# Kernel optimization log

Hardware: AMD Instinct MI355X
Metric: run time of the kernel (lower is better)

The kernel has to match this reference:

```python
import jax, jax.numpy as jnp
import numpy as np

N = 50000   # nodes
E = 600000  # edges (both relations mixed)
D = 128     # in_features == out_features


def _gcn(x, W, b, row, col, w, n):
    """PyG GCNConv: add self-loops (weight 1), symmetric normalization, linear, aggregate, bias.
    Edges with w==0 contribute nothing to degree or messages (== masked subgraph)."""
    idx = jnp.arange(n)
    srow = jnp.concatenate([row, idx])
    scol = jnp.concatenate([col, idx])
    sw = jnp.concatenate([w, jnp.ones((n,), x.dtype)])
    deg = jax.ops.segment_sum(sw, scol, num_segments=n)                 # [n]
    dinv = jnp.where(deg > 0, jax.lax.rsqrt(jnp.maximum(deg, 1e-12)), 0.0)
    norm = dinv[srow] * sw * dinv[scol]                                 # [E+n]
    h = x @ W                                                           # [n, D]
    out = jax.ops.segment_sum(h[srow] * norm[:, None], scol, num_segments=n)
    return out + b


def setup_inputs() -> dict:
    key = jax.random.key(0)
    ks = jax.random.split(key, 12)
    s_in = 1.0 / np.sqrt(D)
    s_g = 1.0 / np.sqrt(3 * D)
    return {
        "x": jax.random.normal(ks[0], (N, D), dtype=jnp.float32),
        "edge_index": jax.random.randint(ks[1], (2, E), 0, N, dtype=jnp.int64),
        "edge_type": jax.random.randint(ks[2], (E,), 0, 2, dtype=jnp.int64),
        "W_sl": jax.random.normal(ks[3], (D, D), dtype=jnp.float32) * s_in,
        "b_sl": jnp.zeros((D,), jnp.float32),
        "W0": jax.random.normal(ks[4], (D, D), dtype=jnp.float32) * s_in,
        "b0": jnp.zeros((D,), jnp.float32),
        "W1": jax.random.normal(ks[5], (D, D), dtype=jnp.float32) * s_in,
        "b1": jnp.zeros((D,), jnp.float32),
        "W_g": jax.random.normal(ks[6], (3 * D, D), dtype=jnp.float32) * s_g,
        "b_g": jnp.zeros((D,), jnp.float32),
    }


def reference(x, edge_index, edge_type, W_sl, b_sl, W0, b0, W1, b1, W_g, b_g):
    n = x.shape[0]
    row, col = edge_index[0], edge_index[1]
    x_x = x @ W_sl + b_sl                                   # self-loop linear
    w0 = (edge_type == 0).astype(x.dtype)
    w1 = (edge_type == 1).astype(x.dtype)
    x_n = _gcn(x, W0, b0, row, col, w0, n)                  # relation 0 GCN
    x_d = _gcn(x, W1, b1, row, col, w1, n)                  # relation 1 GCN
    gat_raw = jax.nn.softmax(jnp.concatenate([x_x, x_n, x_d], axis=1) @ W_g + b_g, axis=-1)
    gat = jnp.cumsum(gat_raw, axis=-1)                      # ordered-neuron gate
    return x_d[:, ::-1] * gat + x_x + x_n
```

## Files before the change

### kernel.cpp

```cpp
#include <hip/hip_runtime.h>
#include <hip/hip_bf16.h>
#include <hip/hip_fp16.h>
#include <math.h>


typedef __attribute__((ext_vector_type(8))) short bf16x8;
typedef __attribute__((ext_vector_type(4))) float f32x4;
typedef __attribute__((ext_vector_type(8))) unsigned short ushort8;

__device__ inline float b2f(unsigned short u) {
  return __uint_as_float(((unsigned)u) << 16);
}
__device__ inline unsigned short f2bf(float f) {
  __hip_bfloat16 b = __float2bfloat16(f);
  return *reinterpret_cast<unsigned short*>(&b);
}

__global__ __launch_bounds__(256) void zero_deg(int4* __restrict__ deg4, int n4) {
  int i = blockIdx.x * 256 + threadIdx.x;
  if (i < n4) deg4[i] = make_int4(0, 0, 0, 0);
}

__global__ __launch_bounds__(256) void pack_count(const float* __restrict__ Wsl,
                                                  const float* __restrict__ W0,
                                                  const float* __restrict__ W1,
                                                  const float* __restrict__ Wg,
                                                  unsigned short* __restrict__ Wp3,
                                                  unsigned short* __restrict__ Wgp,
                                                  const int* __restrict__ col,
                                                  const int* __restrict__ etype,
                                                  int* __restrict__ deg,
                                                  int* __restrict__ erank, int E, int n) {
  if (blockIdx.x < 48) {
    int tid = blockIdx.x * 256 + threadIdx.x;
    if (tid < 6144) {
      int z = tid / 2048, r = tid % 2048;
      int lane = r & 63, idx = r >> 6;
      int kf = idx & 3, ct = idx >> 2;
      const float* W = (z == 0) ? Wsl : (z == 1) ? W0 : W1;
      unsigned short* dst = Wp3 + (size_t)z * 16384 + (size_t)r * 8;
      int krow = kf * 32 + (lane >> 4) * 8;
      int ccol = ct * 16 + (lane & 15);
#pragma unroll
      for (int j = 0; j < 8; ++j) dst[j] = f2bf(W[(size_t)(krow + j) * 128 + ccol]);
    } else {
      int r = tid - 6144;
      int lane = r & 63, idx = r >> 6;
      int kf = idx % 12, ct = idx / 12;
      unsigned short* dst = Wgp + (size_t)r * 8;
      int krow = kf * 32 + (lane >> 4) * 8;
      int ccol = ct * 16 + (lane & 15);
#pragma unroll
      for (int j = 0; j < 8; ++j) dst[j] = f2bf(Wg[(size_t)(krow + j) * 128 + ccol]);
    }
  } else {
    int e = (blockIdx.x - 48) * 256 + threadIdx.x;
    if (e >= E) return;
    int rk = atomicAdd(&deg[(size_t)etype[e] * n + col[e]], 1);
    erank[e] = rk;
  }
}

__global__ __launch_bounds__(256) void scan1(const int* __restrict__ deg,
                                             int* __restrict__ partials, int n2) {
  int tid = threadIdx.x;
  int base = blockIdx.x * 2048 + tid * 8;
  int s = 0;
#pragma unroll
  for (int k = 0; k < 8; ++k) {
    int i = base + k;
    if (i < n2) s += deg[i];
  }
  __shared__ int sb[256];
  sb[tid] = s;
  __syncthreads();
  for (int o = 128; o; o >>= 1) {
    if (tid < o) sb[tid] += sb[tid + o];
    __syncthreads();
  }
  if (tid == 0) partials[blockIdx.x] = sb[0];
}

__global__ __launch_bounds__(256) void scan3b(const int* __restrict__ partials,
                                              const int* __restrict__ deg,
                                              int* __restrict__ row_start,
                                              float* __restrict__ dinv, int n2, int nb) {
  __shared__ int sb[256];
  __shared__ int ex[256];
  int tid = threadIdx.x;
  int pv = (tid < nb) ? partials[tid] : 0;
  sb[tid] = pv;
  __syncthreads();
  for (int o = 1; o < 256; o <<= 1) {
    int t = (tid >= o) ? sb[tid - o] : 0;
    __syncthreads();
    sb[tid] += t;
    __syncthreads();
  }
  ex[tid] = sb[tid] - pv;
  __syncthreads();
  int base = ex[blockIdx.x];
  __syncthreads();

  int bstart = blockIdx.x * 2048 + tid * 8;
  int v[8];
  int s = 0;
#pragma unroll
  for (int k = 0; k < 8; ++k) {
    int i = bstart + k;
    v[k] = (i < n2) ? deg[i] : 0;
    s += v[k];
    if (i < n2) dinv[i] = rsqrtf((float)v[k] + 1.0f);
  }
  sb[tid] = s;
  __syncthreads();
  for (int o = 1; o < 256; o <<= 1) {
    int t = (tid >= o) ? sb[tid - o] : 0;
    __syncthreads();
    sb[tid] += t;
    __syncthreads();
  }
  int run = base + (sb[tid] - s);
#pragma unroll
  for (int k = 0; k < 8; ++k) {
    int i = bstart + k;
    if (i < n2) {
      row_start[i] = run;
      run += v[k];
    }
  }
}

__global__ __launch_bounds__(256) void gemm3_fill(
    const float* __restrict__ x, const unsigned short* __restrict__ Wp3,
    const float* __restrict__ bsl, unsigned short* __restrict__ hx,
    unsigned short* __restrict__ h0, unsigned short* __restrict__ h1,
    const int* __restrict__ row, const int* __restrict__ col,
    const int* __restrict__ etype, const int* __restrict__ erank,
    const int* __restrict__ row_start, const float* __restrict__ dinv,
    unsigned int* __restrict__ ebuf, int n, int E, int gb) {
  __shared__ unsigned short xs[64 * 136];
  __shared__ __align__(16) unsigned short Bs[2][4096];
  int tid = threadIdx.x;
  if ((int)blockIdx.x >= gb) {
    int e = (blockIdx.x - gb) * 256 + tid;
    if (e >= E) return;
    int r = row[e], c = col[e], t = etype[e];
    int b = t * n + c;
    float nrm = dinv[t * n + r] * dinv[b];
    int pos = row_start[b] + erank[e];
    unsigned int rec = (unsigned int)(r & 0xFFFF) |
                       ((unsigned int)__half_as_ushort(__float2half_rn(nrm)) << 16);
    ebuf[pos] = rec;
    return;
  }
  int row0 = blockIdx.x * 64;
  {
    const float4* xg = (const float4*)(x + (size_t)row0 * 128);
    int maxv = (n - row0) * 32;
#pragma unroll
    for (int i = 0; i < 8; ++i) {
      int idx = tid + i * 256;
      float4 v = {0.f, 0.f, 0.f, 0.f};
      if (idx < maxv) v = xg[idx];
      int rr = idx >> 5, c4 = idx & 31;
      ushort4 u;
      u.x = f2bf(v.x);
      u.y = f2bf(v.y);
      u.z = f2bf(v.z);
      u.w = f2bf(v.w);
      *(ushort4*)&xs[rr * 136 + c4 * 4] = u;
    }
    int u = tid;
#pragma unroll
    for (int r = 0; r < 2; ++r, u += 256) {
      int ct = u >> 6, ll = u & 63;
      *(ushort8*)&Bs[0][u * 8] = *(const ushort8*)(Wp3 + ((size_t)(ct * 4) * 64 + ll) * 8);
    }
  }
  __syncthreads();
  int w = tid >> 6;
  int l = tid & 63;
  int q = l >> 4;
  int c = l & 15;
  bf16x8 af[4];
#pragma unroll
  for (int kf = 0; kf < 4; ++kf)
    af[kf] = *(const bf16x8*)&xs[(w * 16 + c) * 136 + kf * 32 + q * 8];
  __syncthreads();

  f32x4 acc[8];
#pragma unroll
  for (int ct = 0; ct < 8; ++ct) acc[ct] = (f32x4){0.f, 0.f, 0.f, 0.f};
#pragma unroll
  for (int g = 0; g < 12; ++g) {
    int z = g >> 2, kf = g & 3;
    int cur = g & 1;
    if (g < 11) {
      int zn = (g + 1) >> 2, kfn = (g + 1) & 3;
      int u = tid;
#pragma unroll
      for (int r = 0; r < 2; ++r, u += 256) {
        int ct = u >> 6, ll = u & 63;
        *(ushort8*)&Bs[cur ^ 1][u * 8] = *(const ushort8*)(
            Wp3 + (size_t)zn * 16384 + ((size_t)(ct * 4 + kfn) * 64 + ll) * 8);
      }
    }
    bf16x8 a = af[kf];
#pragma unroll
    for (int ct = 0; ct < 8; ++ct)
      acc[ct] = __builtin_amdgcn_mfma_f32_16x16x32_bf16(
          a, *(const bf16x8*)&Bs[cur][(ct * 64 + l) * 8], acc[ct], 0, 0, 0);
    if (kf == 3) {
      unsigned short* h = (z == 0) ? hx : (z == 1) ? h0 : h1;
#pragma unroll
      for (int ct = 0; ct < 8; ++ct) {
        int fc = ct * 16 + c;
        float bias = (z == 0) ? bsl[fc] : 0.f;
#pragma unroll
        for (int i = 0; i < 4; ++i)
          xs[(w * 16 + q * 4 + i) * 136 + fc] = f2bf(acc[ct][i] + bias);
        acc[ct] = (f32x4){0.f, 0.f, 0.f, 0.f};
      }
      __syncthreads();
#pragma unroll
      for (int i = 0; i < 4; ++i) {
        int idx = tid + i * 256;
        int rr = idx >> 4, c8 = idx & 15;
        int gr = row0 + rr;
        if (gr < n)
          *(ushort8*)(h + (size_t)gr * 128 + c8 * 8) = *(const ushort8*)&xs[rr * 136 + c8 * 8];
      }
      __syncthreads();
    } else {
      __syncthreads();
    }
  }
}

__global__ __launch_bounds__(256) void gather2(const unsigned short* __restrict__ h0,
                                               const unsigned short* __restrict__ h1,
                                               const unsigned int* __restrict__ ebuf,
                                               const int* __restrict__ row_start,
                                               const int* __restrict__ deg,
                                               const float* __restrict__ dinv,
                                               const float* __restrict__ b0,
                                               const float* __restrict__ b1,
                                               unsigned short* __restrict__ xn,
                                               unsigned short* __restrict__ xd, int n) {
  int t = blockIdx.y;
  long long gid = (long long)blockIdx.x * 256 + threadIdx.x;
  int node = (int)(gid >> 3);
  if (node >= n) return;
  int sub = (int)(gid & 7);
  const ushort8* hp8 = (const ushort8*)(t ? h1 : h0);
  const float* bias = t ? b1 : b0;
  unsigned short* out = t ? xd : xn;
  const int* rs = row_start + (size_t)t * n;
  const int* dg = deg + (size_t)t * n;
  float di = dinv[(size_t)t * n + node];

  float accA[8], accB[8];
  float acc2A[8] = {0, 0, 0, 0, 0, 0, 0, 0}, acc2B[8] = {0, 0, 0, 0, 0, 0, 0, 0};
  {
    ushort8 sa = hp8[(size_t)node * 16 + sub * 2];
    ushort8 sbv = hp8[(size_t)node * 16 + sub * 2 + 1];
    float sl = di * di;
#pragma unroll
    for (int k = 0; k < 8; ++k) {
      accA[k] = fmaf(b2f(sa[k]), sl, bias[sub * 16 + k]);
      accB[k] = fmaf(b2f(sbv[k]), sl, bias[sub * 16 + 8 + k]);
    }
  }
  int s = rs[node];
  int e = s + dg[node];
  int j = s;
  for (; j + 3 < e; j += 4) {
    unsigned int r0 = ebuf[j], r1 = ebuf[j + 1], r2 = ebuf[j + 2], r3 = ebuf[j + 3];
    int i0 = (int)(r0 & 0xFFFFu), i1 = (int)(r1 & 0xFFFFu);
    int i2 = (int)(r2 & 0xFFFFu), i3 = (int)(r3 & 0xFFFFu);
    float n0 = __half2float(__ushort_as_half((unsigned short)(r0 >> 16)));
    float n1 = __half2float(__ushort_as_half((unsigned short)(r1 >> 16)));
    float n2 = __half2float(__ushort_as_half((unsigned short)(r2 >> 16)));
    float n3 = __half2float(__ushort_as_half((unsigned short)(r3 >> 16)));
    ushort8 v0a = hp8[(size_t)i0 * 16 + sub * 2];
    ushort8 v0b = hp8[(size_t)i0 * 16 + sub * 2 + 1];
    ushort8 v1a = hp8[(size_t)i1 * 16 + sub * 2];
    ushort8 v1b = hp8[(size_t)i1 * 16 + sub * 2 + 1];
    ushort8 v2a = hp8[(size_t)i2 * 16 + sub * 2];
    ushort8 v2b = hp8[(size_t)i2 * 16 + sub * 2 + 1];
    ushort8 v3a = hp8[(size_t)i3 * 16 + sub * 2];
    ushort8 v3b = hp8[(size_t)i3 * 16 + sub * 2 + 1];
#pragma unroll
    for (int k = 0; k < 8; ++k) {
      accA[k] = fmaf(b2f(v0a[k]), n0, accA[k]);
      accB[k] = fmaf(b2f(v0b[k]), n0, accB[k]);
      acc2A[k] = fmaf(b2f(v1a[k]), n1, acc2A[k]);
      acc2B[k] = fmaf(b2f(v1b[k]), n1, acc2B[k]);
      accA[k] = fmaf(b2f(v2a[k]), n2, accA[k]);
      accB[k] = fmaf(b2f(v2b[k]), n2, accB[k]);
      acc2A[k] = fmaf(b2f(v3a[k]), n3, acc2A[k]);
      acc2B[k] = fmaf(b2f(v3b[k]), n3, acc2B[k]);
    }
  }
  for (; j < e; ++j) {
    unsigned int r0 = ebuf[j];
    int i0 = (int)(r0 & 0xFFFFu);
    float n0 = __half2float(__ushort_as_half((unsigned short)(r0 >> 16)));
    ushort8 v0a = hp8[(size_t)i0 * 16 + sub * 2];
    ushort8 v0b = hp8[(size_t)i0 * 16 + sub * 2 + 1];
#pragma unroll
    for (int k = 0; k < 8; ++k) {
      accA[k] = fmaf(b2f(v0a[k]), n0, accA[k]);
      accB[k] = fmaf(b2f(v0b[k]), n0, accB[k]);
    }
  }
  ushort8 ua, ub;
#pragma unroll
  for (int k = 0; k < 8; ++k) {
    ua[k] = f2bf(accA[k] + acc2A[k]);
    ub[k] = f2bf(accB[k] + acc2B[k]);
  }
  ((ushort8*)out)[(size_t)node * 16 + sub * 2] = ua;
  ((ushort8*)out)[(size_t)node * 16 + sub * 2 + 1] = ub;
}

__global__ __launch_bounds__(256) void gate_combine(
    const unsigned short* __restrict__ hx, const unsigned short* __restrict__ xn,
    const unsigned short* __restrict__ xd, const unsigned short* __restrict__ Wgp,
    const float* __restrict__ bg, float* __restrict__ out, int n) {
  __shared__ __align__(16) unsigned short Bs[2][4096];
  int tid = threadIdx.x;
  int wv = tid >> 6;
  int l = tid & 63;
  int q = l >> 4;
  int c = l & 15;
  int row0 = blockIdx.x * 64 + wv * 16;
  int ar = row0 + c;
  if (ar > n - 1) ar = n - 1;
  bf16x8 af[12];
  {
    const unsigned short* p0 = hx + (size_t)ar * 128 + q * 8;
    const unsigned short* p1 = xn + (size_t)ar * 128 + q * 8;
    const unsigned short* p2 = xd + (size_t)ar * 128 + q * 8;
#pragma unroll
    for (int k = 0; k < 4; ++k) {
      af[k] = *(const bf16x8*)(p0 + k * 32);
      af[4 + k] = *(const bf16x8*)(p1 + k * 32);
      af[8 + k] = *(const bf16x8*)(p2 + k * 32);
    }
  }
  {
    int u = tid;
#pragma unroll
    for (int r = 0; r < 2; ++r, u += 256) {
      int ct = u >> 6, ll = u & 63;
      *(ushort8*)&Bs[0][u * 8] = *(const ushort8*)(Wgp + ((size_t)(ct * 12) * 64 + ll) * 8);
    }
  }
  __syncthreads();
  f32x4 acc[8];
#pragma unroll
  for (int ct = 0; ct < 8; ++ct) acc[ct] = (f32x4){0.f, 0.f, 0.f, 0.f};
#pragma unroll
  for (int kf = 0; kf < 12; ++kf) {
    int cur = kf & 1;
    if (kf < 11) {
      int u = tid;
#pragma unroll
      for (int r = 0; r < 2; ++r, u += 256) {
        int ct = u >> 6, ll = u & 63;
        *(ushort8*)&Bs[cur ^ 1][u * 8] =
            *(const ushort8*)(Wgp + ((size_t)(ct * 12 + kf + 1) * 64 + ll) * 8);
      }
    }
    bf16x8 a = af[kf];
#pragma unroll
    for (int ct = 0; ct < 8; ++ct)
      acc[ct] = __builtin_amdgcn_mfma_f32_16x16x32_bf16(
          a, *(const bf16x8*)&Bs[cur][(ct * 64 + l) * 8], acc[ct], 0, 0, 0);
    if (kf < 11) __syncthreads();
  }
#pragma unroll
  for (int ct = 0; ct < 8; ++ct) {
    float bgv = bg[ct * 16 + c];
#pragma unroll
    for (int i = 0; i < 4; ++i) acc[ct][i] += bgv;
  }
#pragma unroll
  for (int i = 0; i < 4; ++i) {
    float m = acc[0][i];
#pragma unroll
    for (int ct = 1; ct < 8; ++ct) m = fmaxf(m, acc[ct][i]);
#pragma unroll
    for (int o = 1; o < 16; o <<= 1) m = fmaxf(m, __shfl_xor(m, o));
    float e[8];
    float s = 0.f;
#pragma unroll
    for (int ct = 0; ct < 8; ++ct) {
      e[ct] = __expf(acc[ct][i] - m);
      s += e[ct];
    }
#pragma unroll
    for (int o = 1; o < 16; o <<= 1) s += __shfl_xor(s, o);
    float inv = 1.0f / s;
    int gr = row0 + q * 4 + i;
    float run = 0.f;
#pragma unroll
    for (int ct = 0; ct < 8; ++ct) {
      float p = e[ct];
#pragma unroll
      for (int o = 1; o < 16; o <<= 1) {
        float t = __shfl_up(p, o);
        if (c >= o) p += t;
      }
      float T = __shfl(p, q * 16 + 15);
      float gat = (run + p) * inv;
      run += T;
      int f = ct * 16 + c;
      if (gr < n) {
        size_t gb = (size_t)gr * 128;
        float xxv = b2f(hx[gb + f]);
        float xnv = b2f(xn[gb + f]);
        float xdv = b2f(xd[gb + 127 - f]);
        out[gb + f] = fmaf(xdv, gat, xxv + xnv);
      }
    }
  }
}

extern "C" void kernel_launch(void* const* d_in, const int* in_sizes, int n_in,
                              void* d_out, int out_size, void* d_ws, size_t ws_size,
                              hipStream_t stream) {
  const float* x = (const float*)d_in[0];
  const int* eidx = (const int*)d_in[1];
  const int* etype = (const int*)d_in[2];
  const float* Wsl = (const float*)d_in[3];
  const float* bsl = (const float*)d_in[4];
  const float* W0 = (const float*)d_in[5];
  const float* b0 = (const float*)d_in[6];
  const float* W1 = (const float*)d_in[7];
  const float* b1 = (const float*)d_in[8];
  const float* Wg = (const float*)d_in[9];
  const float* bg = (const float*)d_in[10];
  int n = in_sizes[0] / 128;
  int E = in_sizes[2];
  const int* row = eidx;
  const int* col = eidx + E;
  int n2 = 2 * n;

  char* w = (char*)d_ws;
  int* deg = (int*)w;             w += (size_t)n2 * 4;
  float* dinv = (float*)w;        w += (size_t)n2 * 4;
  int* row_start = (int*)w;       w += (size_t)n2 * 4;
  int* partials = (int*)w;        w += 1024;
  unsigned int* ebuf = (unsigned int*)w;  w += (size_t)E * 4;
  int* erank = (int*)w;           w += (size_t)E * 4;
  unsigned short* Wp3 = (unsigned short*)w;  w += 3 * 128 * 128 * 2;
  unsigned short* Wgp = (unsigned short*)w;  w += 384 * 128 * 2;
  unsigned short* hx = (unsigned short*)w;   w += (size_t)n * 128 * 2;
  unsigned short* h0 = (unsigned short*)w;   w += (size_t)n * 128 * 2;
  unsigned short* h1 = (unsigned short*)w;   w += (size_t)n * 128 * 2;
  unsigned short* xn = (unsigned short*)w;   w += (size_t)n * 128 * 2;
  unsigned short* xd = (unsigned short*)w;
  float* out = (float*)d_out;

  int n4 = n2 / 4;
  zero_deg<<<(n4 + 255) / 256, 256, 0, stream>>>((int4*)deg, n4);

  int cd_blocks = (E + 255) / 256;
  pack_count<<<48 + cd_blocks, 256, 0, stream>>>(Wsl, W0, W1, Wg, Wp3, Wgp,
                                                 col, etype, deg, erank, E, n);
  int nb = (n2 + 2047) / 2048;
  scan1<<<nb, 256, 0, stream>>>(deg, partials, n2);
  scan3b<<<nb, 256, 0, stream>>>(partials, deg, row_start, dinv, n2, nb);

  int gemm_blocks = (n + 63) / 64;
  gemm3_fill<<<gemm_blocks + cd_blocks, 256, 0, stream>>>(
      x, Wp3, bsl, hx, h0, h1, row, col, etype, erank, row_start, dinv, ebuf,
      n, E, gemm_blocks);

  int ga_blocks = (int)(((long long)n * 8 + 255) / 256);
  gather2<<<dim3(ga_blocks, 2), 256, 0, stream>>>(h0, h1, ebuf, row_start, deg, dinv,
                                                  b0, b1, xn, xd, n);
  gate_combine<<<(n + 63) / 64, 256, 0, stream>>>(hx, xn, xd, Wgp, bg, out, n);
}
```

Before: 128.9 us.

## Regroup kernels: fuse degree zeroing with weight packing, edge counting with GEMM

Weight packing now runs in the same launch as zeroing the degree array. Edge degree counting moves into the projection GEMM launch, so the atomic counting overlaps the GEMM. The CSR fill becomes its own kernel after the scans. Kernel count stays the same, but the long count phase now runs alongside GEMM work instead of alone. The cost is a short standalone fill kernel.

```diff
diff --git a/kernel.cpp b/kernel.cpp
--- a/kernel.cpp
+++ b/kernel.cpp
@@ -16,21 +16,13 @@
   return *reinterpret_cast<unsigned short*>(&b);
 }
 
-__global__ __launch_bounds__(256) void zero_deg(int4* __restrict__ deg4, int n4) {
-  int i = blockIdx.x * 256 + threadIdx.x;
-  if (i < n4) deg4[i] = make_int4(0, 0, 0, 0);
-}
-
-__global__ __launch_bounds__(256) void pack_count(const float* __restrict__ Wsl,
-                                                  const float* __restrict__ W0,
-                                                  const float* __restrict__ W1,
-                                                  const float* __restrict__ Wg,
-                                                  unsigned short* __restrict__ Wp3,
-                                                  unsigned short* __restrict__ Wgp,
-                                                  const int* __restrict__ col,
-                                                  const int* __restrict__ etype,
-                                                  int* __restrict__ deg,
-                                                  int* __restrict__ erank, int E, int n) {
+__global__ __launch_bounds__(256) void pack_zero(const float* __restrict__ Wsl,
+                                                 const float* __restrict__ W0,
+                                                 const float* __restrict__ W1,
+                                                 const float* __restrict__ Wg,
+                                                 unsigned short* __restrict__ Wp3,
+                                                 unsigned short* __restrict__ Wgp,
+                                                 int4* __restrict__ deg4, int n4) {
   if (blockIdx.x < 48) {
     int tid = blockIdx.x * 256 + threadIdx.x;
     if (tid < 6144) {
@@ -54,104 +46,25 @@
       for (int j = 0; j < 8; ++j) dst[j] = f2bf(Wg[(size_t)(krow + j) * 128 + ccol]);
     }
   } else {
-    int e = (blockIdx.x - 48) * 256 + threadIdx.x;
-    if (e >= E) return;
-    int rk = atomicAdd(&deg[(size_t)etype[e] * n + col[e]], 1);
-    erank[e] = rk;
-  }
-}
-
-__global__ __launch_bounds__(256) void scan1(const int* __restrict__ deg,
-                                             int* __restrict__ partials, int n2) {
-  int tid = threadIdx.x;
-  int base = blockIdx.x * 2048 + tid * 8;
-  int s = 0;
-#pragma unroll
-  for (int k = 0; k < 8; ++k) {
-    int i = base + k;
-    if (i < n2) s += deg[i];
-  }
-  __shared__ int sb[256];
-  sb[tid] = s;
-  __syncthreads();
-  for (int o = 128; o; o >>= 1) {
-    if (tid < o) sb[tid] += sb[tid + o];
-    __syncthreads();
-  }
-  if (tid == 0) partials[blockIdx.x] = sb[0];
-}
-
-__global__ __launch_bounds__(256) void scan3b(const int* __restrict__ partials,
-                                              const int* __restrict__ deg,
-                                              int* __restrict__ row_start,
-                                              float* __restrict__ dinv, int n2, int nb) {
-  __shared__ int sb[256];
-  __shared__ int ex[256];
-  int tid = threadIdx.x;
-  int pv = (tid < nb) ? partials[tid] : 0;
-  sb[tid] = pv;
-  __syncthreads();
-  for (int o = 1; o < 256; o <<= 1) {
-    int t = (tid >= o) ? sb[tid - o] : 0;
-    __syncthreads();
-    sb[tid] += t;
-    __syncthreads();
-  }
-  ex[tid] = sb[tid] - pv;
-  __syncthreads();
-  int base = ex[blockIdx.x];
-  __syncthreads();
-
-  int bstart = blockIdx.x * 2048 + tid * 8;
-  int v[8];
-  int s = 0;
-#pragma unroll
-  for (int k = 0; k < 8; ++k) {
-    int i = bstart + k;
-    v[k] = (i < n2) ? deg[i] : 0;
-    s += v[k];
-    if (i < n2) dinv[i] = rsqrtf((float)v[k] + 1.0f);
-  }
-  sb[tid] = s;
-  __syncthreads();
-  for (int o = 1; o < 256; o <<= 1) {
-    int t = (tid >= o) ? sb[tid - o] : 0;
-    __syncthreads();
-    sb[tid] += t;
-    __syncthreads();
-  }
-  int run = base + (sb[tid] - s);
-#pragma unroll
-  for (int k = 0; k < 8; ++k) {
-    int i = bstart + k;
-    if (i < n2) {
-      row_start[i] = run;
-      run += v[k];
-    }
-  }
-}
-
-__global__ __launch_bounds__(256) void gemm3_fill(
+    int i = (blockIdx.x - 48) * 256 + threadIdx.x;
+    if (i < n4) deg4[i] = make_int4(0, 0, 0, 0);
+  }
+}
+
+__global__ __launch_bounds__(256) void count_gemm(
     const float* __restrict__ x, const unsigned short* __restrict__ Wp3,
     const float* __restrict__ bsl, unsigned short* __restrict__ hx,
     unsigned short* __restrict__ h0, unsigned short* __restrict__ h1,
-    const int* __restrict__ row, const int* __restrict__ col,
-    const int* __restrict__ etype, const int* __restrict__ erank,
-    const int* __restrict__ row_start, const float* __restrict__ dinv,
-    unsigned int* __restrict__ ebuf, int n, int E, int gb) {
+    const int* __restrict__ col, const int* __restrict__ etype,
+    int* __restrict__ deg, int* __restrict__ erank, int n, int E, int gb) {
   __shared__ unsigned short xs[64 * 136];
   __shared__ __align__(16) unsigned short Bs[2][4096];
   int tid = threadIdx.x;
   if ((int)blockIdx.x >= gb) {
     int e = (blockIdx.x - gb) * 256 + tid;
     if (e >= E) return;
-    int r = row[e], c = col[e], t = etype[e];
-    int b = t * n + c;
-    float nrm = dinv[t * n + r] * dinv[b];
-    int pos = row_start[b] + erank[e];
-    unsigned int rec = (unsigned int)(r & 0xFFFF) |
-                       ((unsigned int)__half_as_ushort(__float2half_rn(nrm)) << 16);
-    ebuf[pos] = rec;
+    int rk = atomicAdd(&deg[(size_t)etype[e] * n + col[e]], 1);
+    erank[e] = rk;
     return;
   }
   int row0 = blockIdx.x * 64;
@@ -236,6 +149,95 @@
       __syncthreads();
     }
   }
+}
+
+__global__ __launch_bounds__(256) void scan1(const int* __restrict__ deg,
+                                             int* __restrict__ partials, int n2) {
+  int tid = threadIdx.x;
+  int base = blockIdx.x * 2048 + tid * 8;
+  int s = 0;
+#pragma unroll
+  for (int k = 0; k < 8; ++k) {
+    int i = base + k;
+    if (i < n2) s += deg[i];
+  }
+  __shared__ int sb[256];
+  sb[tid] = s;
+  __syncthreads();
+  for (int o = 128; o; o >>= 1) {
+    if (tid < o) sb[tid] += sb[tid + o];
+    __syncthreads();
+  }
+  if (tid == 0) partials[blockIdx.x] = sb[0];
+}
+
+__global__ __launch_bounds__(256) void scan3b(const int* __restrict__ partials,
+                                              const int* __restrict__ deg,
+                                              int* __restrict__ row_start,
+                                              float* __restrict__ dinv, int n2, int nb) {
+  __shared__ int sb[256];
+  __shared__ int ex[256];
+  int tid = threadIdx.x;
+  int pv = (tid < nb) ? partials[tid] : 0;
+  sb[tid] = pv;
+  __syncthreads();
+  for (int o = 1; o < 256; o <<= 1) {
+    int t = (tid >= o) ? sb[tid - o] : 0;
+    __syncthreads();
+    sb[tid] += t;
+    __syncthreads();
+  }
+  ex[tid] = sb[tid] - pv;
+  __syncthreads();
+  int base = ex[blockIdx.x];
+  __syncthreads();
+
+  int bstart = blockIdx.x * 2048 + tid * 8;
+  int v[8];
+  int s = 0;
+#pragma unroll
+  for (int k = 0; k < 8; ++k) {
+    int i = bstart + k;
+    v[k] = (i < n2) ? deg[i] : 0;
+    s += v[k];
+    if (i < n2) dinv[i] = rsqrtf((float)v[k] + 1.0f);
+  }
+  sb[tid] = s;
+  __syncthreads();
+  for (int o = 1; o < 256; o <<= 1) {
+    int t = (tid >= o) ? sb[tid - o] : 0;
+    __syncthreads();
+    sb[tid] += t;
+    __syncthreads();
+  }
+  int run = base + (sb[tid] - s);
+#pragma unroll
+  for (int k = 0; k < 8; ++k) {
+    int i = bstart + k;
+    if (i < n2) {
+      row_start[i] = run;
+      run += v[k];
+    }
+  }
+}
+
+__global__ __launch_bounds__(256) void fill_k(const int* __restrict__ row,
+                                              const int* __restrict__ col,
+                                              const int* __restrict__ etype,
+                                              const int* __restrict__ erank,
+                                              const int* __restrict__ row_start,
+                                              const float* __restrict__ dinv,
+                                              unsigned int* __restrict__ ebuf,
+                                              int n, int E) {
+  int e = blockIdx.x * 256 + threadIdx.x;
+  if (e >= E) return;
+  int r = row[e], c = col[e], t = etype[e];
+  int b = t * n + c;
+  float nrm = dinv[t * n + r] * dinv[b];
+  int pos = row_start[b] + erank[e];
+  unsigned int rec = (unsigned int)(r & 0xFFFF) |
+                     ((unsigned int)__half_as_ushort(__float2half_rn(nrm)) << 16);
+  ebuf[pos] = rec;
 }
 
 __global__ __launch_bounds__(256) void gather2(const unsigned short* __restrict__ h0,
@@ -466,19 +468,20 @@
   float* out = (float*)d_out;
 
   int n4 = n2 / 4;
-  zero_deg<<<(n4 + 255) / 256, 256, 0, stream>>>((int4*)deg, n4);
+  int zb = (n4 + 255) / 256;
+  pack_zero<<<48 + zb, 256, 0, stream>>>(Wsl, W0, W1, Wg, Wp3, Wgp, (int4*)deg, n4);
 
   int cd_blocks = (E + 255) / 256;
-  pack_count<<<48 + cd_blocks, 256, 0, stream>>>(Wsl, W0, W1, Wg, Wp3, Wgp,
-                                                 col, etype, deg, erank, E, n);
+  int gemm_blocks = (n + 63) / 64;
+  count_gemm<<<gemm_blocks + cd_blocks, 256, 0, stream>>>(
+      x, Wp3, bsl, hx, h0, h1, col, etype, deg, erank, n, E, gemm_blocks);
+
   int nb = (n2 + 2047) / 2048;
   scan1<<<nb, 256, 0, stream>>>(deg, partials, n2);
   scan3b<<<nb, 256, 0, stream>>>(partials, deg, row_start, dinv, n2, nb);
 
-  int gemm_blocks = (n + 63) / 64;
-  gemm3_fill<<<gemm_blocks + cd_blocks, 256, 0, stream>>>(
-      x, Wp3, bsl, hx, h0, h1, row, col, etype, erank, row_start, dinv, ebuf,
-      n, E, gemm_blocks);
+  fill_k<<<cd_blocks, 256, 0, stream>>>(row, col, etype, erank, row_start, dinv,
+                                        ebuf, n, E);
 
   int ga_blocks = (int)(((long long)n * 8 + 255) / 256);
   gather2<<<dim3(ga_blocks, 2), 256, 0, stream>>>(h0, h1, ebuf, row_start, deg, dinv,
```

Measured after the change: 124.1 us (median of 2 runs). -3.7%, faster.
